# Kernel tuning notes

Measured on AMD Instinct MI355X. Metric: run time of the kernel, lower is better.

## Reference

```python
import jax, jax.numpy as jnp
import numpy as np
import math

B_, V_, D_, N_, H_, W_ = 4, 8, 64, 16, 32, 32
V_LIST = [0.0, 45.0, 90.0, 135.0, 180.0, 225.0, 270.0, 315.0]
GROUPS = 4
EPS = 1e-5


def _make_sample_coords():
    # Replicates F.affine_grid(align_corners=False) for fixed rotation matrices,
    # then maps normalized grid coords to input pixel coords as grid_sample does.
    xs = (np.arange(W_) + 0.5) * 2.0 / W_ - 1.0
    ys = (np.arange(H_) + 0.5) * 2.0 / H_ - 1.0
    X, Y = np.meshgrid(xs, ys)  # (H, W)
    ix_list, iy_list = [], []
    for w in V_LIST:
        a = math.radians(-w)
        c, s = math.cos(a), math.sin(a)
        gx = c * X - s * Y  # theta = [[c,-s,0],[s,c,0]]
        gy = s * X + c * Y
        ix_list.append((gx + 1.0) * W_ / 2.0 - 0.5)
        iy_list.append((gy + 1.0) * H_ / 2.0 - 0.5)
    return (jnp.asarray(np.stack(ix_list), jnp.float32),
            jnp.asarray(np.stack(iy_list), jnp.float32))

IX, IY = _make_sample_coords()  # each (V, H, W)


def _bilinear(sv, iy, ix):
    # sv: (B, D, N, H, W); iy, ix: (H, W) float sampling coords (pixel space)
    x0 = jnp.floor(ix)
    y0 = jnp.floor(iy)
    wx1 = ix - x0
    wy1 = iy - y0

    def corner(yc, xc, wgt):
        m = (yc >= 0) & (yc < H_) & (xc >= 0) & (xc < W_)  # zeros padding
        yi = jnp.clip(yc, 0, H_ - 1).astype(jnp.int32)
        xi = jnp.clip(xc, 0, W_ - 1).astype(jnp.int32)
        return sv[..., yi, xi] * jnp.where(m, wgt, 0.0)

    return (corner(y0, x0, (1.0 - wy1) * (1.0 - wx1))
            + corner(y0, x0 + 1.0, (1.0 - wy1) * wx1)
            + corner(y0 + 1.0, x0, wy1 * (1.0 - wx1))
            + corner(y0 + 1.0, x0 + 1.0, wy1 * wx1))

# vmap over the velocity axis V of s_prev and the per-velocity grids
_transport = jax.vmap(_bilinear, in_axes=(1, 0, 0), out_axes=1)


def _conv(x, w, b=None):
    y = jax.lax.conv_general_dilated(x, w, (1, 1), 'SAME',
                                     dimension_numbers=('NCHW', 'OIHW', 'NCHW'))
    if b is not None:
        y = y + b[None, :, None, None]
    return y


def _group_norm(x, w, b):
    Bn, D, H, W = x.shape
    xg = x.reshape(Bn, GROUPS, D // GROUPS, H, W)
    mu = xg.mean(axis=(2, 3, 4), keepdims=True)
    var = xg.var(axis=(2, 3, 4), keepdims=True)
    xn = ((xg - mu) * jax.lax.rsqrt(var + EPS)).reshape(Bn, D, H, W)
    return xn * w[None, :, None, None] + b[None, :, None, None]


def setup_inputs() -> dict:
    key = jax.random.key(0)
    ks = jax.random.split(key, 5)
    return {
        "u_t": jax.random.normal(ks[0], (B_, D_, H_, W_), jnp.float32),
        "s_prev": jax.random.normal(ks[1], (B_, V_, D_, N_, H_, W_), jnp.float32) * 0.1,
        "gn_w": jnp.ones((D_,), jnp.float32),
        "gn_b": jnp.zeros((D_,), jnp.float32),
        "conv_delta_w": jax.random.normal(ks[2], (D_, D_, 3, 3), jnp.float32) * 0.02,
        "conv_delta_b": jnp.zeros((D_,), jnp.float32),
        "conv_B_w": jax.random.normal(ks[3], (N_, D_, 3, 3), jnp.float32) * 0.02,
        "conv_C_w": jax.random.normal(ks[4], (N_, D_, 3, 3), jnp.float32) * 0.02,
        "log_A_real": jnp.full((D_, N_), math.log(0.5), jnp.float32),
        "D_param": jnp.ones((D_,), jnp.float32),
        "dt_bias": jnp.float32(math.log(math.e - 1.0)),
    }


def reference(u_t, s_prev, gn_w, gn_b, conv_delta_w, conv_delta_b,
              conv_B_w, conv_C_w, log_A_real, D_param, dt_bias):
    u_norm = _group_norm(u_t, gn_w, gn_b)
    delta = jax.nn.softplus(_conv(u_norm, conv_delta_w, conv_delta_b) + dt_bias)
    delta = jnp.clip(delta, 1e-4, 5.0)                               # (B,D,H,W)
    B_val = _conv(u_norm, conv_B_w)                                  # (B,N,H,W)
    C_val = _conv(u_norm, conv_C_w)                                  # (B,N,H,W)
    A = -jnp.exp(log_A_real)                                         # (D,N)
    A_bar = jnp.exp(delta[:, :, None] * A[None, :, :, None, None])   # (B,D,N,H,W)
    B_bar = delta[:, :, None] * B_val[:, None]                       # (B,D,N,H,W)
    s_trans = _transport(s_prev, IY, IX)                             # (B,V,D,N,H,W)
    s_new = A_bar[:, None] * s_trans + B_bar[:, None] * u_t[:, None, :, None]
    y_state = jnp.einsum('bvdnhw,bnhw->bvdhw', s_new, C_val)
    y_new = y_state + u_t[:, None] * D_param[None, None, :, None, None]
    return (y_new, s_new)
```

## Files before the change

kernel.cpp:

```cpp
#include <hip/hip_runtime.h>
#include <cmath>

#define FSQ 0.70710678118654752440f
__constant__ float CTAB[8] = {1.f,  FSQ, 0.f, -FSQ, -1.f, -FSQ, 0.f, FSQ};
__constant__ float STAB[8] = {0.f, -FSQ, -1.f, -FSQ,  0.f,  FSQ, 1.f, FSQ};

__global__ __launch_bounds__(256) void gn_kernel(const float* __restrict__ u,
                                                 const float* __restrict__ gw,
                                                 const float* __restrict__ gb,
                                                 float* __restrict__ up)
{
    int blk = blockIdx.x;
    int b = blk >> 2, g = blk & 3;
    int t = threadIdx.x;
    const float* src = u + ((size_t)(b * 64 + g * 16) << 10);
    float sum = 0.f, sq = 0.f;
    #pragma unroll
    for (int r = 0; r < 64; ++r) {
        float v = src[t + (r << 8)];
        sum += v; sq += v * v;
    }
    __shared__ float red[256], red2[256];
    red[t] = sum; red2[t] = sq;
    __syncthreads();
    for (int ofs = 128; ofs > 0; ofs >>= 1) {
        if (t < ofs) { red[t] += red[t + ofs]; red2[t] += red2[t + ofs]; }
        __syncthreads();
    }
    float mu  = red[0] * (1.f / 16384.f);
    float var = red2[0] * (1.f / 16384.f) - mu * mu;
    float rs  = rsqrtf(var + 1e-5f);

    float* pb = up + (size_t)(b * 64 + g * 16) * 1156;
    for (int k = t; k < 16 * 132; k += 256) {
        int pl = k / 132, c = k % 132;
        int idx;
        if (c < 34)       idx = c;
        else if (c < 68)  idx = 33 * 34 + (c - 34);
        else if (c < 100) idx = (c - 68 + 1) * 34;
        else              idx = (c - 100 + 1) * 34 + 33;
        pb[pl * 1156 + idx] = 0.f;
    }
    for (int r = 0; r < 64; ++r) {
        int idx = t + (r << 8);
        int ch = idx >> 10, rem = idx & 1023;
        int y = rem >> 5, x = rem & 31;
        float val = (src[idx] - mu) * rs * gw[g * 16 + ch] + gb[g * 16 + ch];
        pb[ch * 1156 + (y + 1) * 34 + (x + 1)] = val;
    }
}

__global__ __launch_bounds__(256) void conv_kernel(const float* __restrict__ up,
                                                   const float* __restrict__ wd,
                                                   const float* __restrict__ bd,
                                                   const float* __restrict__ wB,
                                                   const float* __restrict__ wC,
                                                   const float* __restrict__ dtb,
                                                   float* __restrict__ delta,
                                                   float* __restrict__ Bv,
                                                   float* __restrict__ Cv)
{
    __shared__ float sin_[64 * 204];
    __shared__ float red[256];
    int blk = blockIdx.x;
    int strip = blk & 7;
    int o = (blk >> 3) & 127; o = o % 96;
    o = ((blk >> 3) - (blk / 768) * 96);
    int b = blk / 768;
    int h0 = strip * 4;
    int t = threadIdx.x;

    const float* plane = up + (size_t)b * 73984;
    for (int idx = t; idx < 13056; idx += 256) {
        int ci = idx / 204;
        int rem = idx - ci * 204;
        sin_[idx] = plane[ci * 1156 + h0 * 34 + rem];
    }
    __syncthreads();

    const float* wsel;
    if (o < 64)      wsel = wd + (size_t)o * 576;
    else if (o < 80) wsel = wB + (size_t)(o - 64) * 576;
    else             wsel = wC + (size_t)(o - 80) * 576;

    int half = t >> 7;
    int px = t & 127;
    int r = px >> 5, c = px & 31;
    const float* base = sin_ + r * 34 + c;

    float acc = 0.f;
    int ci0 = half * 32;
    for (int ci = ci0; ci < ci0 + 32; ++ci) {
        const float* pp = base + ci * 204;
        const float* wp = wsel + ci * 9;
        #pragma unroll
        for (int dy = 0; dy < 3; ++dy)
            #pragma unroll
            for (int dx = 0; dx < 3; ++dx)
                acc += pp[dy * 34 + dx] * wp[dy * 3 + dx];
    }
    red[t] = acc;
    __syncthreads();
    if (t < 128) {
        float a = red[t] + red[t + 128];
        int pidx = (h0 + r) * 32 + c;
        if (o < 64) {
            float x = a + bd[o] + dtb[0];
            float sp = (x > 20.f) ? x : log1pf(expf(x));
            sp = fminf(fmaxf(sp, 1e-4f), 5.f);
            delta[((size_t)(b * 64 + o) << 10) + pidx] = sp;
        } else if (o < 80) {
            Bv[((size_t)(b * 16 + o - 64) << 10) + pidx] = a;
        } else {
            Cv[((size_t)(b * 16 + o - 80) << 10) + pidx] = a;
        }
    }
}

__global__ __launch_bounds__(256) void fused_state_kernel(
    const float* __restrict__ s_prev, const float* __restrict__ u_t,
    const float* __restrict__ delta, const float* __restrict__ Bv,
    const float* __restrict__ Cv, const float* __restrict__ logA,
    const float* __restrict__ Dp, float* __restrict__ y_out,
    float* __restrict__ s_out)
{
    __shared__ float lds[8 * 1156];
    __shared__ float Ash[8];
    int blk = blockIdx.x;
    int cchunk = blk & 1;
    int d = (blk >> 1) & 63, v = (blk >> 7) & 7, b = blk >> 10;
    int t = threadIdx.x;

    if (t < 8) Ash[t] = -__expf(logA[d * 16 + cchunk * 8 + t]);
    for (int k = t; k < 1056; k += 256) {
        int pl = k >> 7; int g = k & 127;
        pl = k / 132; g = k - pl * 132;
        int idx;
        if (g < 34)       idx = g;
        else if (g < 68)  idx = 1122 + (g - 34);
        else if (g < 100) idx = (g - 67) * 34;
        else              idx = (g - 99) * 34 + 33;
        lds[pl * 1156 + idx] = 0.f;
    }

    size_t so = (((size_t)((b * 8 + v) * 64 + d)) << 14) + (cchunk << 13);
    const float4* src = (const float4*)(s_prev + so);
    #pragma unroll
    for (int k = 0; k < 8; ++k) {
        int q = t + (k << 8);
        float4 val = src[q];
        int lin = q << 2;
        int nn = lin >> 10, rem = lin & 1023;
        int di = nn * 1156 + ((rem >> 5) + 1) * 34 + (rem & 31) + 1;
        lds[di] = val.x; lds[di + 1] = val.y; lds[di + 2] = val.z; lds[di + 3] = val.w;
    }
    __syncthreads();

    const float cc = CTAB[v], ss = STAB[v];
    const float* dpl = delta + ((size_t)(b * 64 + d) << 10);
    const float* upl = u_t   + ((size_t)(b * 64 + d) << 10);
    const float* bvc = Bv + ((size_t)b << 14) + (cchunk << 13);
    const float* cvc = Cv + ((size_t)b << 14) + (cchunk << 13);
    float* soc = s_out + so;
    float* yo  = y_out + (((size_t)((b * 8 + v) * 64 + d)) << 10);
    float Dd = Dp[d];

    for (int i = 0; i < 4; ++i) {
        int p = t + (i << 8);
        int h = p >> 5, wpx = p & 31;
        float X = (wpx + 0.5f) * 0.0625f - 1.f;
        float Y = (h + 0.5f) * 0.0625f - 1.f;
        float gx = cc * X - ss * Y;
        float gy = ss * X + cc * Y;
        float ix = (gx + 1.f) * 16.f - 0.5f;
        float iy = (gy + 1.f) * 16.f - 0.5f;
        float fx0 = floorf(ix), fy0 = floorf(iy);
        float wx = ix - fx0, wy = iy - fy0;
        int x0 = (int)fx0, y0 = (int)fy0;
        float mx0 = (x0 >= 0 && x0 < 32) ? (1.f - wx) : 0.f;
        float mx1 = (x0 >= -1 && x0 < 31) ? wx : 0.f;
        float my0 = (y0 >= 0 && y0 < 32) ? (1.f - wy) : 0.f;
        float my1 = (y0 >= -1 && y0 < 31) ? wy : 0.f;
        float w00 = my0 * mx0, w01 = my0 * mx1;
        float w10 = my1 * mx0, w11 = my1 * mx1;
        int bx = min(max(x0, -1), 31), by = min(max(y0, -1), 31);
        int base = (by + 1) * 34 + (bx + 1);

        float dd = dpl[p], uv = upl[p];
        float du = dd * uv;
        float yacc = 0.f;
        #pragma unroll
        for (int nn = 0; nn < 8; ++nn) {
            int si = base + nn * 1156;
            float s00 = lds[si], s01 = lds[si + 1];
            float s10 = lds[si + 34], s11 = lds[si + 35];
            float bil = s00 * w00 + s01 * w01 + s10 * w10 + s11 * w11;
            float abar = __expf(dd * Ash[nn]);
            float bvv = bvc[(nn << 10) + p];
            float sn = abar * bil + du * bvv;
            soc[(nn << 10) + p] = sn;
            yacc += sn * cvc[(nn << 10) + p];
        }
        float val = yacc + (cchunk == 0 ? uv * Dd : 0.f);
        atomicAdd(yo + p, val);
    }
}

extern "C" void kernel_launch(void* const* d_in, const int* in_sizes, int n_in,
                              void* d_out, int out_size, void* d_ws, size_t ws_size,
                              hipStream_t stream)
{
    const float* u_t    = (const float*)d_in[0];
    const float* s_prev = (const float*)d_in[1];
    const float* gn_w   = (const float*)d_in[2];
    const float* gn_b   = (const float*)d_in[3];
    const float* wd     = (const float*)d_in[4];
    const float* bd     = (const float*)d_in[5];
    const float* wB     = (const float*)d_in[6];
    const float* wC     = (const float*)d_in[7];
    const float* logA   = (const float*)d_in[8];
    const float* Dp     = (const float*)d_in[9];
    const float* dtb    = (const float*)d_in[10];

    float* y_out = (float*)d_out;
    float* s_out = y_out + 2097152;

    float* up    = (float*)d_ws;
    float* delta = up + 295936;
    float* Bv    = delta + 262144;
    float* Cv    = Bv + 65536;

    hipMemsetAsync(y_out, 0, (size_t)2097152 * sizeof(float), stream);

    hipLaunchKernelGGL(gn_kernel, dim3(16), dim3(256), 0, stream, u_t, gn_w, gn_b, up);
    hipLaunchKernelGGL(conv_kernel, dim3(3072), dim3(256), 0, stream,
                       up, wd, bd, wB, wC, dtb, delta, Bv, Cv);
    hipLaunchKernelGGL(fused_state_kernel, dim3(4096), dim3(256), 0, stream,
                       s_prev, u_t, delta, Bv, Cv, logA, Dp, y_out, s_out);
}
```

Before: 319.6 us.

## Rework all three kernels: wave-shuffle GN, 4-output conv blocks, single-block state chunks

GroupNorm now uses 1024 threads per block and reduces with wave shuffles instead of a shared-memory tree. The conv kernel computes four output channels per block, reusing each loaded input tile four times, and launches a quarter as many blocks. The state kernel now handles both N-chunks in one block. It prefetches the second chunk into registers while computing the first, which removes the y memset and the atomicAdds. The trade-off is higher register pressure and fewer blocks in the conv and state kernels.

```diff
diff --git a/kernel.cpp b/kernel.cpp
--- a/kernel.cpp
+++ b/kernel.cpp
@@ -5,10 +5,10 @@
 __constant__ float CTAB[8] = {1.f,  FSQ, 0.f, -FSQ, -1.f, -FSQ, 0.f, FSQ};
 __constant__ float STAB[8] = {0.f, -FSQ, -1.f, -FSQ,  0.f,  FSQ, 1.f, FSQ};
 
-__global__ __launch_bounds__(256) void gn_kernel(const float* __restrict__ u,
-                                                 const float* __restrict__ gw,
-                                                 const float* __restrict__ gb,
-                                                 float* __restrict__ up)
+__global__ __launch_bounds__(1024) void gn_kernel(const float* __restrict__ u,
+                                                  const float* __restrict__ gw,
+                                                  const float* __restrict__ gb,
+                                                  float* __restrict__ up)
 {
     int blk = blockIdx.x;
     int b = blk >> 2, g = blk & 3;
@@ -16,24 +16,29 @@
     const float* src = u + ((size_t)(b * 64 + g * 16) << 10);
     float sum = 0.f, sq = 0.f;
     #pragma unroll
-    for (int r = 0; r < 64; ++r) {
-        float v = src[t + (r << 8)];
+    for (int r = 0; r < 16; ++r) {
+        float v = src[t + (r << 10)];
         sum += v; sq += v * v;
     }
-    __shared__ float red[256], red2[256];
-    red[t] = sum; red2[t] = sq;
-    __syncthreads();
-    for (int ofs = 128; ofs > 0; ofs >>= 1) {
-        if (t < ofs) { red[t] += red[t + ofs]; red2[t] += red2[t + ofs]; }
-        __syncthreads();
-    }
-    float mu  = red[0] * (1.f / 16384.f);
-    float var = red2[0] * (1.f / 16384.f) - mu * mu;
+    #pragma unroll
+    for (int ofs = 32; ofs > 0; ofs >>= 1) {
+        sum += __shfl_down(sum, ofs);
+        sq  += __shfl_down(sq, ofs);
+    }
+    __shared__ float red[16], red2[16];
+    int wv = t >> 6;
+    if ((t & 63) == 0) { red[wv] = sum; red2[wv] = sq; }
+    __syncthreads();
+    float s_tot = 0.f, q_tot = 0.f;
+    #pragma unroll
+    for (int k = 0; k < 16; ++k) { s_tot += red[k]; q_tot += red2[k]; }
+    float mu  = s_tot * (1.f / 16384.f);
+    float var = q_tot * (1.f / 16384.f) - mu * mu;
     float rs  = rsqrtf(var + 1e-5f);
 
     float* pb = up + (size_t)(b * 64 + g * 16) * 1156;
-    for (int k = t; k < 16 * 132; k += 256) {
-        int pl = k / 132, c = k % 132;
+    for (int k = t; k < 16 * 132; k += 1024) {
+        int pl = k / 132, c = k - pl * 132;
         int idx;
         if (c < 34)       idx = c;
         else if (c < 68)  idx = 33 * 34 + (c - 34);
@@ -41,12 +46,11 @@
         else              idx = (c - 100 + 1) * 34 + 33;
         pb[pl * 1156 + idx] = 0.f;
     }
-    for (int r = 0; r < 64; ++r) {
-        int idx = t + (r << 8);
-        int ch = idx >> 10, rem = idx & 1023;
-        int y = rem >> 5, x = rem & 31;
-        float val = (src[idx] - mu) * rs * gw[g * 16 + ch] + gb[g * 16 + ch];
-        pb[ch * 1156 + (y + 1) * 34 + (x + 1)] = val;
+    int y = t >> 5, x = t & 31;
+    #pragma unroll
+    for (int r = 0; r < 16; ++r) {
+        float val = (src[t + (r << 10)] - mu) * rs * gw[g * 16 + r] + gb[g * 16 + r];
+        pb[r * 1156 + (y + 1) * 34 + (x + 1)] = val;
     }
 }
 
@@ -61,12 +65,10 @@
                                                    float* __restrict__ Cv)
 {
     __shared__ float sin_[64 * 204];
-    __shared__ float red[256];
     int blk = blockIdx.x;
     int strip = blk & 7;
-    int o = (blk >> 3) & 127; o = o % 96;
-    o = ((blk >> 3) - (blk / 768) * 96);
-    int b = blk / 768;
+    int og = (blk >> 3) % 24;
+    int b = blk / 192;
     int h0 = strip * 4;
     int t = threadIdx.x;
 
@@ -78,17 +80,18 @@
     }
     __syncthreads();
 
+    int o0 = og * 4;
     const float* wsel;
-    if (o < 64)      wsel = wd + (size_t)o * 576;
-    else if (o < 80) wsel = wB + (size_t)(o - 64) * 576;
-    else             wsel = wC + (size_t)(o - 80) * 576;
+    if (o0 < 64)      wsel = wd + (size_t)o0 * 576;
+    else if (o0 < 80) wsel = wB + (size_t)(o0 - 64) * 576;
+    else              wsel = wC + (size_t)(o0 - 80) * 576;
 
     int half = t >> 7;
     int px = t & 127;
     int r = px >> 5, c = px & 31;
     const float* base = sin_ + r * 34 + c;
 
-    float acc = 0.f;
+    float acc0 = 0.f, acc1 = 0.f, acc2 = 0.f, acc3 = 0.f;
     int ci0 = half * 32;
     for (int ci = ci0; ci < ci0 + 32; ++ci) {
         const float* pp = base + ci * 204;
@@ -96,28 +99,45 @@
         #pragma unroll
         for (int dy = 0; dy < 3; ++dy)
             #pragma unroll
-            for (int dx = 0; dx < 3; ++dx)
-                acc += pp[dy * 34 + dx] * wp[dy * 3 + dx];
-    }
-    red[t] = acc;
+            for (int dx = 0; dx < 3; ++dx) {
+                float v = pp[dy * 34 + dx];
+                int wi = dy * 3 + dx;
+                acc0 += v * wp[wi];
+                acc1 += v * wp[576 + wi];
+                acc2 += v * wp[1152 + wi];
+                acc3 += v * wp[1728 + wi];
+            }
+    }
+    __syncthreads();
+    float4* red4 = (float4*)sin_;
+    red4[t] = make_float4(acc0, acc1, acc2, acc3);
     __syncthreads();
     if (t < 128) {
-        float a = red[t] + red[t + 128];
+        float4 a = red4[t], bq = red4[t + 128];
+        float s0 = a.x + bq.x, s1 = a.y + bq.y, s2 = a.z + bq.z, s3 = a.w + bq.w;
+        float s[4] = {s0, s1, s2, s3};
         int pidx = (h0 + r) * 32 + c;
-        if (o < 64) {
-            float x = a + bd[o] + dtb[0];
-            float sp = (x > 20.f) ? x : log1pf(expf(x));
-            sp = fminf(fmaxf(sp, 1e-4f), 5.f);
-            delta[((size_t)(b * 64 + o) << 10) + pidx] = sp;
-        } else if (o < 80) {
-            Bv[((size_t)(b * 16 + o - 64) << 10) + pidx] = a;
+        if (o0 < 64) {
+            #pragma unroll
+            for (int k = 0; k < 4; ++k) {
+                float x = s[k] + bd[o0 + k] + dtb[0];
+                float sp = (x > 20.f) ? x : log1pf(expf(x));
+                sp = fminf(fmaxf(sp, 1e-4f), 5.f);
+                delta[((size_t)(b * 64 + o0 + k) << 10) + pidx] = sp;
+            }
+        } else if (o0 < 80) {
+            #pragma unroll
+            for (int k = 0; k < 4; ++k)
+                Bv[((size_t)(b * 16 + o0 - 64 + k) << 10) + pidx] = s[k];
         } else {
-            Cv[((size_t)(b * 16 + o - 80) << 10) + pidx] = a;
+            #pragma unroll
+            for (int k = 0; k < 4; ++k)
+                Cv[((size_t)(b * 16 + o0 - 80 + k) << 10) + pidx] = s[k];
         }
     }
 }
 
-__global__ __launch_bounds__(256) void fused_state_kernel(
+__global__ __launch_bounds__(256, 4) void fused_state_kernel(
     const float* __restrict__ s_prev, const float* __restrict__ u_t,
     const float* __restrict__ delta, const float* __restrict__ Bv,
     const float* __restrict__ Cv, const float* __restrict__ logA,
@@ -125,16 +145,14 @@
     float* __restrict__ s_out)
 {
     __shared__ float lds[8 * 1156];
-    __shared__ float Ash[8];
+    __shared__ float Ash[16];
     int blk = blockIdx.x;
-    int cchunk = blk & 1;
-    int d = (blk >> 1) & 63, v = (blk >> 7) & 7, b = blk >> 10;
+    int d = blk & 63, v = (blk >> 6) & 7, b = blk >> 9;
     int t = threadIdx.x;
 
-    if (t < 8) Ash[t] = -__expf(logA[d * 16 + cchunk * 8 + t]);
+    if (t < 16) Ash[t] = -__expf(logA[d * 16 + t]);
     for (int k = t; k < 1056; k += 256) {
-        int pl = k >> 7; int g = k & 127;
-        pl = k / 132; g = k - pl * 132;
+        int pl = k / 132, g = k - pl * 132;
         int idx;
         if (g < 34)       idx = g;
         else if (g < 68)  idx = 1122 + (g - 34);
@@ -143,28 +161,36 @@
         lds[pl * 1156 + idx] = 0.f;
     }
 
-    size_t so = (((size_t)((b * 8 + v) * 64 + d)) << 14) + (cchunk << 13);
-    const float4* src = (const float4*)(s_prev + so);
+    size_t so = ((size_t)((b * 8 + v) * 64 + d)) << 14;
+    const float4* src0 = (const float4*)(s_prev + so);
+    const float4* src1 = (const float4*)(s_prev + so + 8192);
+
+    float4 rg[8];
+    #pragma unroll
+    for (int k = 0; k < 8; ++k) rg[k] = src0[t + (k << 8)];
     #pragma unroll
     for (int k = 0; k < 8; ++k) {
         int q = t + (k << 8);
-        float4 val = src[q];
         int lin = q << 2;
         int nn = lin >> 10, rem = lin & 1023;
         int di = nn * 1156 + ((rem >> 5) + 1) * 34 + (rem & 31) + 1;
-        lds[di] = val.x; lds[di + 1] = val.y; lds[di + 2] = val.z; lds[di + 3] = val.w;
-    }
-    __syncthreads();
+        lds[di] = rg[k].x; lds[di + 1] = rg[k].y; lds[di + 2] = rg[k].z; lds[di + 3] = rg[k].w;
+    }
+    __syncthreads();
+    #pragma unroll
+    for (int k = 0; k < 8; ++k) rg[k] = src1[t + (k << 8)];
 
     const float cc = CTAB[v], ss = STAB[v];
     const float* dpl = delta + ((size_t)(b * 64 + d) << 10);
     const float* upl = u_t   + ((size_t)(b * 64 + d) << 10);
-    const float* bvc = Bv + ((size_t)b << 14) + (cchunk << 13);
-    const float* cvc = Cv + ((size_t)b << 14) + (cchunk << 13);
     float* soc = s_out + so;
     float* yo  = y_out + (((size_t)((b * 8 + v) * 64 + d)) << 10);
     float Dd = Dp[d];
 
+    float dd[4], uv[4], du[4], yacc[4];
+    float w00[4], w01[4], w10[4], w11[4];
+    int tbase[4];
+    #pragma unroll
     for (int i = 0; i < 4; ++i) {
         int p = t + (i << 8);
         int h = p >> 5, wpx = p & 31;
@@ -181,28 +207,67 @@
         float mx1 = (x0 >= -1 && x0 < 31) ? wx : 0.f;
         float my0 = (y0 >= 0 && y0 < 32) ? (1.f - wy) : 0.f;
         float my1 = (y0 >= -1 && y0 < 31) ? wy : 0.f;
-        float w00 = my0 * mx0, w01 = my0 * mx1;
-        float w10 = my1 * mx0, w11 = my1 * mx1;
+        w00[i] = my0 * mx0; w01[i] = my0 * mx1;
+        w10[i] = my1 * mx0; w11[i] = my1 * mx1;
         int bx = min(max(x0, -1), 31), by = min(max(y0, -1), 31);
-        int base = (by + 1) * 34 + (bx + 1);
-
-        float dd = dpl[p], uv = upl[p];
-        float du = dd * uv;
-        float yacc = 0.f;
+        tbase[i] = (by + 1) * 34 + (bx + 1);
+        dd[i] = dpl[p]; uv[i] = upl[p]; du[i] = dd[i] * uv[i];
+        yacc[i] = 0.f;
+    }
+
+    {
+        const float* bvc = Bv + ((size_t)b << 14);
+        const float* cvc = Cv + ((size_t)b << 14);
         #pragma unroll
-        for (int nn = 0; nn < 8; ++nn) {
-            int si = base + nn * 1156;
-            float s00 = lds[si], s01 = lds[si + 1];
-            float s10 = lds[si + 34], s11 = lds[si + 35];
-            float bil = s00 * w00 + s01 * w01 + s10 * w10 + s11 * w11;
-            float abar = __expf(dd * Ash[nn]);
-            float bvv = bvc[(nn << 10) + p];
-            float sn = abar * bil + du * bvv;
-            soc[(nn << 10) + p] = sn;
-            yacc += sn * cvc[(nn << 10) + p];
+        for (int i = 0; i < 4; ++i) {
+            int p = t + (i << 8);
+            #pragma unroll
+            for (int nn = 0; nn < 8; ++nn) {
+                int si = tbase[i] + nn * 1156;
+                float s00 = lds[si], s01 = lds[si + 1];
+                float s10 = lds[si + 34], s11 = lds[si + 35];
+                float bil = s00 * w00[i] + s01 * w01[i] + s10 * w10[i] + s11 * w11[i];
+                float abar = __expf(dd[i] * Ash[nn]);
+                float sn = abar * bil + du[i] * bvc[(nn << 10) + p];
+                soc[(nn << 10) + p] = sn;
+                yacc[i] += sn * cvc[(nn << 10) + p];
+            }
         }
-        float val = yacc + (cchunk == 0 ? uv * Dd : 0.f);
-        atomicAdd(yo + p, val);
+    }
+    __syncthreads();
+    #pragma unroll
+    for (int k = 0; k < 8; ++k) {
+        int q = t + (k << 8);
+        int lin = q << 2;
+        int nn = lin >> 10, rem = lin & 1023;
+        int di = nn * 1156 + ((rem >> 5) + 1) * 34 + (rem & 31) + 1;
+        lds[di] = rg[k].x; lds[di + 1] = rg[k].y; lds[di + 2] = rg[k].z; lds[di + 3] = rg[k].w;
+    }
+    __syncthreads();
+    {
+        const float* bvc = Bv + ((size_t)b << 14) + 8192;
+        const float* cvc = Cv + ((size_t)b << 14) + 8192;
+        float* soc1 = soc + 8192;
+        #pragma unroll
+        for (int i = 0; i < 4; ++i) {
+            int p = t + (i << 8);
+            #pragma unroll
+            for (int nn = 0; nn < 8; ++nn) {
+                int si = tbase[i] + nn * 1156;
+                float s00 = lds[si], s01 = lds[si + 1];
+                float s10 = lds[si + 34], s11 = lds[si + 35];
+                float bil = s00 * w00[i] + s01 * w01[i] + s10 * w10[i] + s11 * w11[i];
+                float abar = __expf(dd[i] * Ash[8 + nn]);
+                float sn = abar * bil + du[i] * bvc[(nn << 10) + p];
+                soc1[(nn << 10) + p] = sn;
+                yacc[i] += sn * cvc[(nn << 10) + p];
+            }
+        }
+    }
+    #pragma unroll
+    for (int i = 0; i < 4; ++i) {
+        int p = t + (i << 8);
+        yo[p] = yacc[i] + uv[i] * Dd;
     }
 }
 
@@ -230,11 +295,9 @@
     float* Bv    = delta + 262144;
     float* Cv    = Bv + 65536;
 
-    hipMemsetAsync(y_out, 0, (size_t)2097152 * sizeof(float), stream);
-
-    hipLaunchKernelGGL(gn_kernel, dim3(16), dim3(256), 0, stream, u_t, gn_w, gn_b, up);
-    hipLaunchKernelGGL(conv_kernel, dim3(3072), dim3(256), 0, stream,
+    hipLaunchKernelGGL(gn_kernel, dim3(16), dim3(1024), 0, stream, u_t, gn_w, gn_b, up);
+    hipLaunchKernelGGL(conv_kernel, dim3(768), dim3(256), 0, stream,
                        up, wd, bd, wB, wC, dtb, delta, Bv, Cv);
-    hipLaunchKernelGGL(fused_state_kernel, dim3(4096), dim3(256), 0, stream,
+    hipLaunchKernelGGL(fused_state_kernel, dim3(2048), dim3(256), 0, stream,
                        s_prev, u_t, delta, Bv, Cv, logA, Dp, y_out, s_out);
 }
```

Result: slower. 410.9 us (+28.6%).
